# Performance work log

Measured on AMD Instinct MI355X. Metric: run time of the kernel, lower is better.

## Reference

```python
import jax, jax.numpy as jnp
from jax import lax
import numpy as np

B, T, D, H, OUT = 128, 1024, 256, 256, 2


def _rnn_layer(inp, W_xh, W_hh, b):
    # inp: [B, T, Din]; returns [B, T, H]
    h0 = jnp.zeros((inp.shape[0], W_hh.shape[0]), inp.dtype)

    def step(h, x_t):
        h_new = jnp.tanh(x_t @ W_xh.T + h @ W_hh.T + b)
        return h_new, h_new

    _, ys = lax.scan(step, h0, jnp.swapaxes(inp, 0, 1))  # ys: [T, B, H]
    return jnp.swapaxes(ys, 0, 1)


def setup_inputs() -> dict:
    key = jax.random.key(0)
    ks = jax.random.split(key, 8)
    s_in = 1.0 / np.sqrt(H)  # torch nn.RNN init scale
    x = jax.random.normal(ks[0], (B, T, D), dtype=jnp.float32)
    W_xh0 = jax.random.uniform(ks[1], (H, D), jnp.float32, -s_in, s_in)
    W_hh0 = jax.random.uniform(ks[2], (H, H), jnp.float32, -s_in, s_in)
    b0 = jax.random.uniform(ks[3], (H,), jnp.float32, -s_in, s_in)
    W_xh1 = jax.random.uniform(ks[4], (H, H), jnp.float32, -s_in, s_in)
    W_hh1 = jax.random.uniform(ks[5], (H, H), jnp.float32, -s_in, s_in)
    b1 = jax.random.uniform(ks[6], (H,), jnp.float32, -s_in, s_in)
    fc_w = jax.random.uniform(ks[7], (OUT, H), jnp.float32, -s_in, s_in)
    fc_b = jnp.zeros((OUT,), jnp.float32)
    return {"x": x, "W_xh0": W_xh0, "W_hh0": W_hh0, "b0": b0,
            "W_xh1": W_xh1, "W_hh1": W_hh1, "b1": b1,
            "fc_w": fc_w, "fc_b": fc_b}


def reference(x, W_xh0, W_hh0, b0, W_xh1, W_hh1, b1, fc_w, fc_b):
    h1 = _rnn_layer(x, W_xh0, W_hh0, b0)   # [B, T, H]
    h2 = _rnn_layer(h1, W_xh1, W_hh1, b1)  # [B, T, H]
    # linear head on last timestep
    return h2[:, -1, :] @ fc_w.T + fc_b    # [B, OUT]
```

## Files before the change

### kernel.cpp

```cpp
#include <hip/hip_runtime.h>

#define Bsz 128
#define Tn  1024
#define Dn  256
#define Hn  256

typedef _Float16 f16;
typedef _Float16 f16x4 __attribute__((ext_vector_type(4)));
typedef _Float16 f16x8 __attribute__((ext_vector_type(8)));
typedef float f32x4 __attribute__((ext_vector_type(4)));

__device__ __forceinline__ float tanh_fast(float x) {
    float e = __builtin_amdgcn_exp2f(x * 2.88539008177793f);
    return 1.0f - 2.0f * __builtin_amdgcn_rcpf(e + 1.0f);
}

__device__ __forceinline__ void wg_barrier() {
    asm volatile("s_waitcnt lgkmcnt(0)\n\ts_barrier" ::: "memory");
}


__global__ __launch_bounds__(256, 2) void k_xproj(
    const float* __restrict__ x, const float* __restrict__ W,
    const float* __restrict__ bias, float* __restrict__ preT)
{
    __shared__ __align__(16) f16 xt[128][264];
    const int tid = threadIdx.x;
    const int t = blockIdx.x;

    for (int i = tid; i < 128 * 64; i += 256) {
        int row = i >> 6, c4 = i & 63;
        float4 v = *(const float4*)(x + ((size_t)row * Tn + t) * Dn + c4 * 4);
        f16x4 tv = { (f16)v.x, (f16)v.y, (f16)v.z, (f16)v.w };
        *(f16x4*)(&xt[row][c4 * 4]) = tv;
    }

    const int lane = tid & 63, l15 = lane & 15, quad = lane >> 4;
    const int w = tid >> 6;

    f16x8 wf[4][8];
    #pragma unroll
    for (int jn = 0; jn < 4; jn++) {
        int j = w * 64 + jn * 16 + l15;
        #pragma unroll
        for (int kk = 0; kk < 8; kk++)
            #pragma unroll
            for (int e = 0; e < 8; e++)
                wf[jn][kk][e] = (f16)W[(size_t)j * Dn + kk * 32 + quad * 8 + e];
    }
    float4 bi[4];
    #pragma unroll
    for (int jn = 0; jn < 4; jn++)
        bi[jn] = *(const float4*)(bias + w * 64 + jn * 16 + quad * 4);

    __syncthreads();

    #pragma unroll 1
    for (int bblk = 0; bblk < 8; bblk++) {
        f32x4 acc[4];
        #pragma unroll
        for (int jn = 0; jn < 4; jn++)
            acc[jn] = (f32x4){bi[jn].x, bi[jn].y, bi[jn].z, bi[jn].w};
        #pragma unroll
        for (int kk = 0; kk < 8; kk++) {
            f16x8 xb = *(const f16x8*)(&xt[bblk * 16 + l15][kk * 32 + quad * 8]);
            #pragma unroll
            for (int jn = 0; jn < 4; jn++)
                acc[jn] = __builtin_amdgcn_mfma_f32_16x16x32_f16(wf[jn][kk], xb, acc[jn], 0, 0, 0);
        }
        #pragma unroll
        for (int jn = 0; jn < 4; jn++)
            #pragma unroll
            for (int r = 0; r < 4; r++) {
                int j = w * 64 + jn * 16 + quad * 4 + r;
                preT[((size_t)t * Hn + j) * Bsz + bblk * 16 + l15] = acc[jn][r];
            }
    }
}

__global__ __launch_bounds__(512, 1) void k_fused(
    const float* __restrict__ Whh0, const float* __restrict__ Wxh1,
    const float* __restrict__ Whh1, const float* __restrict__ b1v,
    const float* __restrict__ fcw,  const float* __restrict__ fcb,
    const float* __restrict__ preT, float* __restrict__ out)
{
    __shared__ __align__(16) f16 h1f[2][4096];
    __shared__ __align__(16) f16 h2f[2][4096];

    const int tid  = threadIdx.x;
    const int lane = tid & 63, l15 = lane & 15, quad = lane >> 4;
    const int w    = tid >> 6;
    const int colbase = w * 32;
    const int bg   = blockIdx.x * 16;

    for (int i = tid; i < 4096; i += 512) {
        h1f[0][i] = (f16)0.0f; h1f[1][i] = (f16)0.0f;
        h2f[0][i] = (f16)0.0f; h2f[1][i] = (f16)0.0f;
    }

    f16x8 wh0[2][8], wx[2][8], wh1[2][8];
    #pragma unroll
    for (int jn = 0; jn < 2; jn++) {
        int j = colbase + jn * 16 + l15;
        #pragma unroll
        for (int kk = 0; kk < 8; kk++)
            #pragma unroll
            for (int e = 0; e < 8; e++) {
                int o = (int)((size_t)j * Hn + kk * 32 + quad * 8 + e);
                wh0[jn][kk][e] = (f16)Whh0[o];
                wx [jn][kk][e] = (f16)Wxh1[o];
                wh1[jn][kk][e] = (f16)Whh1[o];
            }
    }
    float4 bi[2];
    #pragma unroll
    for (int jn = 0; jn < 2; jn++)
        bi[jn] = *(const float4*)(b1v + colbase + jn * 16 + quad * 4);

    int wroff[2];
    int pbase[2];
    #pragma unroll
    for (int jn = 0; jn < 2; jn++) {
        int n0 = colbase + jn * 16 + quad * 4;
        wroff[jn] = (n0 >> 5) * 512 + ((n0 >> 3) & 3) * 128 + l15 * 8 + (n0 & 7);
        pbase[jn] = n0 * Bsz + bg + l15;
    }

    float pn[8];
    #pragma unroll
    for (int jn = 0; jn < 2; jn++)
        #pragma unroll
        for (int r = 0; r < 4; r++)
            pn[jn * 4 + r] = preT[pbase[jn] + r * Bsz];
    __syncthreads();

#define FSTEP_FULL(PR, I, TF) { \
    f32x4 accA[2], accB[2]; \
    _Pragma("unroll") for (int jn = 0; jn < 2; jn++) { \
        _Pragma("unroll") for (int r = 0; r < 4; r++) accA[jn][r] = pn[jn*4+r]; \
        accB[jn] = (f32x4){bi[jn].x, bi[jn].y, bi[jn].z, bi[jn].w}; \
    } \
    _Pragma("unroll") for (int jn = 0; jn < 2; jn++) \
        _Pragma("unroll") for (int r = 0; r < 4; r++) \
            pn[jn*4+r] = preT[(size_t)(TF) * (Hn * Bsz) + pbase[jn] + r * Bsz]; \
    _Pragma("unroll") for (int kk = 0; kk < 8; kk++) { \
        f16x8 hb1 = *(const f16x8*)(&h1f[(PR)^1][kk * 512 + lane * 8]); \
        f16x8 hb2 = *(const f16x8*)(&h2f[(PR)  ][kk * 512 + lane * 8]); \
        accA[0] = __builtin_amdgcn_mfma_f32_16x16x32_f16(wh0[0][kk], hb1, accA[0], 0, 0, 0); \
        accA[1] = __builtin_amdgcn_mfma_f32_16x16x32_f16(wh0[1][kk], hb1, accA[1], 0, 0, 0); \
        accB[0] = __builtin_amdgcn_mfma_f32_16x16x32_f16(wx [0][kk], hb1, accB[0], 0, 0, 0); \
        accB[1] = __builtin_amdgcn_mfma_f32_16x16x32_f16(wx [1][kk], hb1, accB[1], 0, 0, 0); \
        accB[0] = __builtin_amdgcn_mfma_f32_16x16x32_f16(wh1[0][kk], hb2, accB[0], 0, 0, 0); \
        accB[1] = __builtin_amdgcn_mfma_f32_16x16x32_f16(wh1[1][kk], hb2, accB[1], 0, 0, 0); \
    } \
    _Pragma("unroll") for (int jn = 0; jn < 2; jn++) { \
        f16x4 t1v = { (f16)tanh_fast(accA[jn][0]), (f16)tanh_fast(accA[jn][1]), \
                      (f16)tanh_fast(accA[jn][2]), (f16)tanh_fast(accA[jn][3]) }; \
        *(f16x4*)(&h1f[(PR)][wroff[jn]]) = t1v; \
        f16x4 t2v = { (f16)tanh_fast(accB[jn][0]), (f16)tanh_fast(accB[jn][1]), \
                      (f16)tanh_fast(accB[jn][2]), (f16)tanh_fast(accB[jn][3]) }; \
        *(f16x4*)(&h2f[(PR)^1][wroff[jn]]) = t2v; \
    } \
    wg_barrier(); \
}

    {
        f32x4 accA[2];
        #pragma unroll
        for (int jn = 0; jn < 2; jn++)
            #pragma unroll
            for (int r = 0; r < 4; r++) accA[jn][r] = pn[jn * 4 + r];
        #pragma unroll
        for (int jn = 0; jn < 2; jn++)
            #pragma unroll
            for (int r = 0; r < 4; r++)
                pn[jn * 4 + r] = preT[(size_t)1 * (Hn * Bsz) + pbase[jn] + r * Bsz];
        #pragma unroll
        for (int kk = 0; kk < 8; kk++) {
            f16x8 hb1 = *(const f16x8*)(&h1f[1][kk * 512 + lane * 8]);
            accA[0] = __builtin_amdgcn_mfma_f32_16x16x32_f16(wh0[0][kk], hb1, accA[0], 0, 0, 0);
            accA[1] = __builtin_amdgcn_mfma_f32_16x16x32_f16(wh0[1][kk], hb1, accA[1], 0, 0, 0);
        }
        #pragma unroll
        for (int jn = 0; jn < 2; jn++) {
            f16x4 t1v = { (f16)tanh_fast(accA[jn][0]), (f16)tanh_fast(accA[jn][1]),
                          (f16)tanh_fast(accA[jn][2]), (f16)tanh_fast(accA[jn][3]) };
            *(f16x4*)(&h1f[0][wroff[jn]]) = t1v;
        }
        wg_barrier();
    }

    #pragma unroll 1
    for (int tp = 0; tp < 511; ++tp) {
        const int t1 = 2 * tp + 1;
        FSTEP_FULL(1, t1, (t1 + 1))
        FSTEP_FULL(0, (t1 + 1), (t1 + 2))
    }
    FSTEP_FULL(1, 1023, 1023)
#undef FSTEP_FULL

    {
        f32x4 accB[2];
        #pragma unroll
        for (int jn = 0; jn < 2; jn++)
            accB[jn] = (f32x4){bi[jn].x, bi[jn].y, bi[jn].z, bi[jn].w};
        #pragma unroll
        for (int kk = 0; kk < 8; kk++) {
            f16x8 hb1 = *(const f16x8*)(&h1f[1][kk * 512 + lane * 8]);
            f16x8 hb2 = *(const f16x8*)(&h2f[0][kk * 512 + lane * 8]);
            accB[0] = __builtin_amdgcn_mfma_f32_16x16x32_f16(wx [0][kk], hb1, accB[0], 0, 0, 0);
            accB[1] = __builtin_amdgcn_mfma_f32_16x16x32_f16(wx [1][kk], hb1, accB[1], 0, 0, 0);
            accB[0] = __builtin_amdgcn_mfma_f32_16x16x32_f16(wh1[0][kk], hb2, accB[0], 0, 0, 0);
            accB[1] = __builtin_amdgcn_mfma_f32_16x16x32_f16(wh1[1][kk], hb2, accB[1], 0, 0, 0);
        }
        #pragma unroll
        for (int jn = 0; jn < 2; jn++) {
            f16x4 t2v = { (f16)tanh_fast(accB[jn][0]), (f16)tanh_fast(accB[jn][1]),
                          (f16)tanh_fast(accB[jn][2]), (f16)tanh_fast(accB[jn][3]) };
            *(f16x4*)(&h2f[1][wroff[jn]]) = t2v;
        }
        wg_barrier();
    }

    if (tid < 256) {
        const int bl = tid >> 4, o = (tid >> 3) & 1, kc = tid & 7;
        float s = 0.f;
        #pragma unroll
        for (int kq = 0; kq < 32; kq++) {
            int k = kc * 32 + kq;
            f16 hv = h2f[1][(k >> 5) * 512 + ((k >> 3) & 3) * 128 + bl * 8 + (k & 7)];
            s += (float)hv * fcw[o * Hn + k];
        }
        s += __shfl_down(s, 4);
        s += __shfl_down(s, 2);
        s += __shfl_down(s, 1);
        if (kc == 0)
            out[(bg + bl) * 2 + o] = s + fcb[o];
    }
}

extern "C" void kernel_launch(void* const* d_in, const int* in_sizes, int n_in,
                              void* d_out, int out_size, void* d_ws, size_t ws_size,
                              hipStream_t stream) {
    const float* x    = (const float*)d_in[0];
    const float* Wxh0 = (const float*)d_in[1];
    const float* Whh0 = (const float*)d_in[2];
    const float* b0   = (const float*)d_in[3];
    const float* Wxh1 = (const float*)d_in[4];
    const float* Whh1 = (const float*)d_in[5];
    const float* b1   = (const float*)d_in[6];
    const float* fcw  = (const float*)d_in[7];
    const float* fcb  = (const float*)d_in[8];
    float* out = (float*)d_out;

    float* preT = (float*)d_ws;

    k_xproj<<<dim3(Tn),       dim3(256), 0, stream>>>(x, Wxh0, b0, preT);
    k_fused<<<dim3(Bsz / 16), dim3(512), 0, stream>>>(Whh0, Wxh1, Whh1, b1,
                                                      fcw, fcb, preT, out);
}
```

Before: 1.438 ms.

## Store projection as [T,B,H] with vector accesses and reorder fused step layers

Changes the precomputed layer-0 input projection layout from [T,H,B] to [T,B,H], so each lane writes and reads a contiguous float4 instead of four strided scalars. The fused recurrent step is also split: the layer-1 h MFMAs, tanh and LDS write run first, then the layer-2 MFMAs reuse the cached h1 fragments. This is meant to cut global load/store instruction count and to get the layer-1 result written earlier in the step. It keeps eight f16x8 h1 fragments live, which raises register pressure in a 512-thread kernel that already holds its weights in registers.

```diff
diff --git a/kernel.cpp b/kernel.cpp
--- a/kernel.cpp
+++ b/kernel.cpp
@@ -69,12 +69,10 @@
                 acc[jn] = __builtin_amdgcn_mfma_f32_16x16x32_f16(wf[jn][kk], xb, acc[jn], 0, 0, 0);
         }
         #pragma unroll
-        for (int jn = 0; jn < 4; jn++)
-            #pragma unroll
-            for (int r = 0; r < 4; r++) {
-                int j = w * 64 + jn * 16 + quad * 4 + r;
-                preT[((size_t)t * Hn + j) * Bsz + bblk * 16 + l15] = acc[jn][r];
-            }
+        for (int jn = 0; jn < 4; jn++) {
+            int j0 = w * 64 + jn * 16 + quad * 4;
+            *(f32x4*)(preT + ((size_t)t * Bsz + bblk * 16 + l15) * Hn + j0) = acc[jn];
+        }
     }
 }
 
@@ -118,45 +116,47 @@
         bi[jn] = *(const float4*)(b1v + colbase + jn * 16 + quad * 4);
 
     int wroff[2];
-    int pbase[2];
     #pragma unroll
     for (int jn = 0; jn < 2; jn++) {
         int n0 = colbase + jn * 16 + quad * 4;
         wroff[jn] = (n0 >> 5) * 512 + ((n0 >> 3) & 3) * 128 + l15 * 8 + (n0 & 7);
-        pbase[jn] = n0 * Bsz + bg + l15;
-    }
-
-    float pn[8];
-    #pragma unroll
-    for (int jn = 0; jn < 2; jn++)
-        #pragma unroll
-        for (int r = 0; r < 4; r++)
-            pn[jn * 4 + r] = preT[pbase[jn] + r * Bsz];
+    }
+
+    const float* pp = preT + ((size_t)(bg + l15)) * Hn + colbase + quad * 4;
+
+    f32x4 pnv[2];
+    pnv[0] = *(const f32x4*)(pp);
+    pnv[1] = *(const f32x4*)(pp + 16);
     __syncthreads();
 
 #define FSTEP_FULL(PR, I, TF) { \
-    f32x4 accA[2], accB[2]; \
-    _Pragma("unroll") for (int jn = 0; jn < 2; jn++) { \
-        _Pragma("unroll") for (int r = 0; r < 4; r++) accA[jn][r] = pn[jn*4+r]; \
-        accB[jn] = (f32x4){bi[jn].x, bi[jn].y, bi[jn].z, bi[jn].w}; \
-    } \
-    _Pragma("unroll") for (int jn = 0; jn < 2; jn++) \
-        _Pragma("unroll") for (int r = 0; r < 4; r++) \
-            pn[jn*4+r] = preT[(size_t)(TF) * (Hn * Bsz) + pbase[jn] + r * Bsz]; \
+    f32x4 accA[2]; \
+    accA[0] = pnv[0]; accA[1] = pnv[1]; \
+    pnv[0] = *(const f32x4*)(pp + (size_t)(TF) * (Bsz * Hn)); \
+    pnv[1] = *(const f32x4*)(pp + (size_t)(TF) * (Bsz * Hn) + 16); \
+    f16x8 hb1[8]; \
     _Pragma("unroll") for (int kk = 0; kk < 8; kk++) { \
-        f16x8 hb1 = *(const f16x8*)(&h1f[(PR)^1][kk * 512 + lane * 8]); \
-        f16x8 hb2 = *(const f16x8*)(&h2f[(PR)  ][kk * 512 + lane * 8]); \
-        accA[0] = __builtin_amdgcn_mfma_f32_16x16x32_f16(wh0[0][kk], hb1, accA[0], 0, 0, 0); \
-        accA[1] = __builtin_amdgcn_mfma_f32_16x16x32_f16(wh0[1][kk], hb1, accA[1], 0, 0, 0); \
-        accB[0] = __builtin_amdgcn_mfma_f32_16x16x32_f16(wx [0][kk], hb1, accB[0], 0, 0, 0); \
-        accB[1] = __builtin_amdgcn_mfma_f32_16x16x32_f16(wx [1][kk], hb1, accB[1], 0, 0, 0); \
-        accB[0] = __builtin_amdgcn_mfma_f32_16x16x32_f16(wh1[0][kk], hb2, accB[0], 0, 0, 0); \
-        accB[1] = __builtin_amdgcn_mfma_f32_16x16x32_f16(wh1[1][kk], hb2, accB[1], 0, 0, 0); \
-    } \
+        hb1[kk] = *(const f16x8*)(&h1f[(PR)^1][kk * 512 + lane * 8]); \
+        accA[0] = __builtin_amdgcn_mfma_f32_16x16x32_f16(wh0[0][kk], hb1[kk], accA[0], 0, 0, 0); \
+        accA[1] = __builtin_amdgcn_mfma_f32_16x16x32_f16(wh0[1][kk], hb1[kk], accA[1], 0, 0, 0); \
+    } \
+     \
     _Pragma("unroll") for (int jn = 0; jn < 2; jn++) { \
         f16x4 t1v = { (f16)tanh_fast(accA[jn][0]), (f16)tanh_fast(accA[jn][1]), \
                       (f16)tanh_fast(accA[jn][2]), (f16)tanh_fast(accA[jn][3]) }; \
         *(f16x4*)(&h1f[(PR)][wroff[jn]]) = t1v; \
+    } \
+    f32x4 accB[2]; \
+    _Pragma("unroll") for (int jn = 0; jn < 2; jn++) \
+        accB[jn] = (f32x4){bi[jn].x, bi[jn].y, bi[jn].z, bi[jn].w}; \
+    _Pragma("unroll") for (int kk = 0; kk < 8; kk++) { \
+        f16x8 hb2 = *(const f16x8*)(&h2f[(PR)][kk * 512 + lane * 8]); \
+        accB[0] = __builtin_amdgcn_mfma_f32_16x16x32_f16(wx [0][kk], hb1[kk], accB[0], 0, 0, 0); \
+        accB[1] = __builtin_amdgcn_mfma_f32_16x16x32_f16(wx [1][kk], hb1[kk], accB[1], 0, 0, 0); \
+        accB[0] = __builtin_amdgcn_mfma_f32_16x16x32_f16(wh1[0][kk], hb2, accB[0], 0, 0, 0); \
+        accB[1] = __builtin_amdgcn_mfma_f32_16x16x32_f16(wh1[1][kk], hb2, accB[1], 0, 0, 0); \
+    } \
+    _Pragma("unroll") for (int jn = 0; jn < 2; jn++) { \
         f16x4 t2v = { (f16)tanh_fast(accB[jn][0]), (f16)tanh_fast(accB[jn][1]), \
                       (f16)tanh_fast(accB[jn][2]), (f16)tanh_fast(accB[jn][3]) }; \
         *(f16x4*)(&h2f[(PR)^1][wroff[jn]]) = t2v; \
@@ -166,15 +166,9 @@
 
     {
         f32x4 accA[2];
-        #pragma unroll
-        for (int jn = 0; jn < 2; jn++)
-            #pragma unroll
-            for (int r = 0; r < 4; r++) accA[jn][r] = pn[jn * 4 + r];
-        #pragma unroll
-        for (int jn = 0; jn < 2; jn++)
-            #pragma unroll
-            for (int r = 0; r < 4; r++)
-                pn[jn * 4 + r] = preT[(size_t)1 * (Hn * Bsz) + pbase[jn] + r * Bsz];
+        accA[0] = pnv[0]; accA[1] = pnv[1];
+        pnv[0] = *(const f32x4*)(pp + (size_t)1 * (Bsz * Hn));
+        pnv[1] = *(const f32x4*)(pp + (size_t)1 * (Bsz * Hn) + 16);
         #pragma unroll
         for (int kk = 0; kk < 8; kk++) {
             f16x8 hb1 = *(const f16x8*)(&h1f[1][kk * 512 + lane * 8]);
```

After: 1.372 ms. 4.6% less time.
